# Kernel optimization log

Hardware: AMD Instinct MI355X
Metric: run time of the kernel (lower is better)

Reference implementation:

```python
import jax, jax.numpy as jnp
import numpy as np

COMMITMENT_COST = 0.25
KLD_SCALE = 1.0


def setup_inputs() -> dict:
    key = jax.random.key(0)
    k1, k2 = jax.random.split(key)
    z = jax.random.normal(k1, (8, 4096, 512), dtype=jnp.float32)
    embed_w = jax.random.normal(k2, (1024, 512), dtype=jnp.float32)
    return {"z": z, "embed_w": embed_w}


def reference(z, embed_w):
    bsz, s, d = z.shape
    flat = z.reshape(-1, d)  # [N, d]
    dist = (
        jnp.sum(flat * flat, axis=1, keepdims=True)
        - 2.0 * flat @ embed_w.T
        + jnp.sum(embed_w * embed_w, axis=1)[None, :]
    )
    ind = jnp.argmin(dist, axis=1).reshape(bsz, s)  # (-dist).max == dist.min
    z_q = embed_w[ind]  # codebook gather [bsz, s, d]
    sg = jax.lax.stop_gradient
    diff = COMMITMENT_COST * ((sg(z_q) - z) ** 2 + (z_q - sg(z)) ** 2)
    diff = diff * KLD_SCALE
    z_q = z + sg(z_q - z)  # straight-through estimator
    return z_q, diff, ind
```

## Files before the change

kernel.cpp:

```cpp
#include <hip/hip_runtime.h>
#include <math.h>


#define D_DIM   512
#define K_CODES 1024
#define N_TOK   32768

#define BM 128
#define BN 128
#define NKT 16

typedef __attribute__((ext_vector_type(8))) short bf16x8;
typedef __attribute__((ext_vector_type(4))) float f32x4;

__device__ __forceinline__ unsigned short bf16_rne(float f) {
    unsigned int u = __float_as_uint(f);
    return (unsigned short)((u + 0x7FFFu + ((u >> 16) & 1u)) >> 16);
}
__device__ __forceinline__ float bf16_to_f32(unsigned short b) {
    return __uint_as_float(((unsigned int)b) << 16);
}

#define GLOAD16(gp, lp)                                                        \
    __builtin_amdgcn_global_load_lds(                                          \
        (const __attribute__((address_space(1))) void*)(gp),                   \
        (__attribute__((address_space(3))) void*)(lp), 16, 0, 0)

__global__ __launch_bounds__(256) void vq_zsplit(const float* __restrict__ z,
                                                 unsigned short* __restrict__ zhi,
                                                 unsigned short* __restrict__ zlo) {
    const int tid = blockIdx.x * 256 + threadIdx.x;
    const float4* z4 = (const float4*)z;
    ushort4* h4 = (ushort4*)zhi;
    ushort4* l4 = (ushort4*)zlo;
#pragma unroll
    for (int g = 0; g < 8; ++g) {
        const size_t i = (size_t)g * 524288 + tid;
        float4 v = z4[i];
        float f[4] = {v.x, v.y, v.z, v.w};
        unsigned short hb[4], lb[4];
#pragma unroll
        for (int j = 0; j < 4; ++j) {
            hb[j] = bf16_rne(f[j]);
            lb[j] = bf16_rne(f[j] - bf16_to_f32(hb[j]));
        }
        h4[i] = make_ushort4(hb[0], hb[1], hb[2], hb[3]);
        l4[i] = make_ushort4(lb[0], lb[1], lb[2], lb[3]);
    }
}

__global__ __launch_bounds__(256) void vq_prep(const float* __restrict__ ew,
                                               unsigned short* __restrict__ ehi,
                                               unsigned short* __restrict__ elo,
                                               float* __restrict__ e2) {
    const int wv = threadIdx.x >> 6, lane = threadIdx.x & 63;
    const int code = blockIdx.x * 4 + wv;
    const float* row = ew + (size_t)code * D_DIM;
    float s = 0.0f;
#pragma unroll
    for (int h = 0; h < 2; ++h) {
        const int c = h * 256 + lane * 4;
        float4 v = *(const float4*)(row + c);
        float f[4] = {v.x, v.y, v.z, v.w};
        unsigned short hb[4], lb[4];
#pragma unroll
        for (int j = 0; j < 4; ++j) {
            s = fmaf(f[j], f[j], s);
            hb[j] = bf16_rne(f[j]);
            lb[j] = bf16_rne(f[j] - bf16_to_f32(hb[j]));
        }
        *(ushort4*)(ehi + (size_t)code * D_DIM + c) = make_ushort4(hb[0], hb[1], hb[2], hb[3]);
        *(ushort4*)(elo + (size_t)code * D_DIM + c) = make_ushort4(lb[0], lb[1], lb[2], lb[3]);
    }
#pragma unroll
    for (int off = 32; off > 0; off >>= 1) s += __shfl_xor(s, off, 64);
    if (lane == 0) e2[code] = s;
}

__global__ __launch_bounds__(256, 2) void vq_gemm(
    const unsigned short* __restrict__ zhi, const unsigned short* __restrict__ zlo,
    const unsigned short* __restrict__ ehi, const unsigned short* __restrict__ elo,
    const float* __restrict__ e2, float* __restrict__ pv, float* __restrict__ pif) {
    __shared__ __align__(16) unsigned short lds[32768];
    const int AHI = 0, ALO = 4096, BHI = 8192, BLO = 12288;

    const int t = threadIdx.x, lane = t & 63, wv = t >> 6;
    const int b  = blockIdx.x;
    const int wg = (b & 7) * 256 + (b >> 3);
    const int mtile = wg >> 3, ntile = wg & 7;
    const int row0 = mtile * BM;
    const int c0g  = ntile * BN;

    const int idx0 = (wv * 2 + 0) * 64 + lane;
    const int idx1 = (wv * 2 + 1) * 64 + lane;
    const int c_0 = idx0 >> 7, r_0 = idx0 & 127;
    const int c_1 = idx1 >> 7, r_1 = idx1 & 127;
    const size_t zo0 = (size_t)(row0 + r_0) * D_DIM + c_0 * 8;
    const size_t zo1 = (size_t)(row0 + r_1) * D_DIM + c_1 * 8;
    const size_t eo0 = (size_t)(c0g + r_0) * D_DIM + c_0 * 8;
    const size_t eo1 = (size_t)(c0g + r_1) * D_DIM + c_1 * 8;
    const int l0 = (wv * 2 + 0) * 512;
    const int l1 = (wv * 2 + 1) * 512;

    const int wr = wv >> 1, wc = wv & 1;
    const int lm = lane & 15, lk = lane >> 4;

    f32x4 acc[4][4];
    const f32x4 zero4 = {0.f, 0.f, 0.f, 0.f};
#pragma unroll
    for (int i = 0; i < 4; ++i)
#pragma unroll
        for (int j = 0; j < 4; ++j) acc[i][j] = zero4;

    auto stage = [&](int kt, int bufo) {
        const int ko = kt * 32;
        GLOAD16(zhi + zo0 + ko, &lds[bufo + AHI + l0]);
        GLOAD16(zhi + zo1 + ko, &lds[bufo + AHI + l1]);
        GLOAD16(zlo + zo0 + ko, &lds[bufo + ALO + l0]);
        GLOAD16(zlo + zo1 + ko, &lds[bufo + ALO + l1]);
        GLOAD16(ehi + eo0 + ko, &lds[bufo + BHI + l0]);
        GLOAD16(ehi + eo1 + ko, &lds[bufo + BHI + l1]);
        GLOAD16(elo + eo0 + ko, &lds[bufo + BLO + l0]);
        GLOAD16(elo + eo1 + ko, &lds[bufo + BLO + l1]);
    };

    auto compute = [&](int bufo) {
        bf16x8 ah[4], al[4], bh[4], bl[4];
#pragma unroll
        for (int mi = 0; mi < 4; ++mi) {
            const int s = (lk * 128 + wr * 64 + mi * 16 + lm) * 8;
            ah[mi] = *(const bf16x8*)&lds[bufo + AHI + s];
            al[mi] = *(const bf16x8*)&lds[bufo + ALO + s];
        }
#pragma unroll
        for (int nj = 0; nj < 4; ++nj) {
            const int s = (lk * 128 + wc * 64 + nj * 16 + lm) * 8;
            bh[nj] = *(const bf16x8*)&lds[bufo + BHI + s];
            bl[nj] = *(const bf16x8*)&lds[bufo + BLO + s];
        }
        __builtin_amdgcn_s_setprio(1);
#pragma unroll
        for (int mi = 0; mi < 4; ++mi)
#pragma unroll
            for (int nj = 0; nj < 4; ++nj)
                acc[mi][nj] = __builtin_amdgcn_mfma_f32_16x16x32_bf16(
                    ah[mi], bh[nj], acc[mi][nj], 0, 0, 0);
#pragma unroll
        for (int mi = 0; mi < 4; ++mi)
#pragma unroll
            for (int nj = 0; nj < 4; ++nj)
                acc[mi][nj] = __builtin_amdgcn_mfma_f32_16x16x32_bf16(
                    ah[mi], bl[nj], acc[mi][nj], 0, 0, 0);
#pragma unroll
        for (int mi = 0; mi < 4; ++mi)
#pragma unroll
            for (int nj = 0; nj < 4; ++nj)
                acc[mi][nj] = __builtin_amdgcn_mfma_f32_16x16x32_bf16(
                    al[mi], bh[nj], acc[mi][nj], 0, 0, 0);
        __builtin_amdgcn_s_setprio(0);
    };

    stage(0, 0);
    stage(1, 16384);

    for (int kt = 0; kt < NKT - 1; ++kt) {
        const int bufo = (kt & 1) * 16384;
        asm volatile("s_waitcnt vmcnt(8)" ::: "memory");
        __builtin_amdgcn_s_barrier();
        __builtin_amdgcn_sched_barrier(0);
        compute(bufo);
        __builtin_amdgcn_sched_barrier(0);
        __builtin_amdgcn_s_barrier();
        if (kt + 2 < NKT) stage(kt + 2, bufo);
    }
    {
        const int bufo = ((NKT - 1) & 1) * 16384;
        asm volatile("s_waitcnt vmcnt(0)" ::: "memory");
        __builtin_amdgcn_s_barrier();
        __builtin_amdgcn_sched_barrier(0);
        compute(bufo);
    }

    float best[16], bidx[16];
#pragma unroll
    for (int i = 0; i < 16; ++i) { best[i] = INFINITY; bidx[i] = 0.f; }
#pragma unroll
    for (int nj = 0; nj < 4; ++nj) {
        const int cloc = wc * 64 + nj * 16 + lm;
        const float e2v = e2[c0g + cloc];
#pragma unroll
        for (int mi = 0; mi < 4; ++mi)
#pragma unroll
            for (int r = 0; r < 4; ++r) {
                const float sc = fmaf(-2.0f, acc[mi][nj][r], e2v);
                const int bi = mi * 4 + r;
                if (sc < best[bi]) { best[bi] = sc; bidx[bi] = (float)(c0g + cloc); }
            }
    }
#pragma unroll
    for (int off = 1; off < 16; off <<= 1) {
#pragma unroll
        for (int bi = 0; bi < 16; ++bi) {
            float v2 = __shfl_xor(best[bi], off, 64);
            float i2 = __shfl_xor(bidx[bi], off, 64);
            if (v2 < best[bi] || (v2 == best[bi] && i2 < bidx[bi])) {
                best[bi] = v2; bidx[bi] = i2;
            }
        }
    }
    __syncthreads();
    float* sv = (float*)lds;
    float* si = sv + 256;
    if (lm == 0) {
#pragma unroll
        for (int mi = 0; mi < 4; ++mi)
#pragma unroll
            for (int r = 0; r < 4; ++r) {
                const int rl = wr * 64 + mi * 16 + lk * 4 + r;
                sv[wc * 128 + rl] = best[mi * 4 + r];
                si[wc * 128 + rl] = bidx[mi * 4 + r];
            }
    }
    __syncthreads();
    if (t < 128) {
        float v0 = sv[t], i0 = si[t];
        float v1 = sv[128 + t], i1 = si[128 + t];
        if (v1 < v0 || (v1 == v0 && i1 < i0)) { v0 = v1; i0 = i1; }
        pv [(size_t)ntile * N_TOK + row0 + t] = v0;
        pif[(size_t)ntile * N_TOK + row0 + t] = i0;
    }
}

__global__ __launch_bounds__(256) void vq_out_kernel(
    const float* __restrict__ z, const float* __restrict__ ew,
    const float* __restrict__ pv, const float* __restrict__ pif,
    float* __restrict__ indf, float* __restrict__ zq, float* __restrict__ diff) {
    const int w    = threadIdx.x >> 6;
    const int lane = threadIdx.x & 63;
    const int row  = blockIdx.x * 4 + w;

    float v = INFINITY, ix = 0.f;
    if (lane < 8) {
        v  = pv [(size_t)lane * N_TOK + row];
        ix = pif[(size_t)lane * N_TOK + row];
    }
#pragma unroll
    for (int off = 1; off < 8; off <<= 1) {
        float v2 = __shfl_xor(v, off, 64);
        float i2 = __shfl_xor(ix, off, 64);
        if (v2 < v || (v2 == v && i2 < ix)) { v = v2; ix = i2; }
    }
    const float ixb = __shfl(ix, 0, 64);
    const int c = (int)ixb;
    if (lane == 0) indf[row] = ixb;

    const float4* z4 = (const float4*)&z[(size_t)row * D_DIM];
    const float4* e4 = (const float4*)&ew[(size_t)c * D_DIM];
    float4* q4 = (float4*)&zq[(size_t)row * D_DIM];
    float4* d4 = (float4*)&diff[(size_t)row * D_DIM];

#pragma unroll
    for (int vv = 0; vv < 2; ++vv) {
        const int i = vv * 64 + lane;
        const float4 zv = z4[i];
        const float4 ev = e4[i];
        float4 qv, dv;
        float ax = ev.x - zv.x, ay = ev.y - zv.y, az = ev.z - zv.z, aw = ev.w - zv.w;
        qv.x = zv.x + ax; qv.y = zv.y + ay; qv.z = zv.z + az; qv.w = zv.w + aw;
        dv.x = 0.5f * (ax * ax); dv.y = 0.5f * (ay * ay);
        dv.z = 0.5f * (az * az); dv.w = 0.5f * (aw * aw);
        q4[i] = qv;
        d4[i] = dv;
    }
}

extern "C" void kernel_launch(void* const* d_in, const int* in_sizes, int n_in,
                              void* d_out, int out_size, void* d_ws, size_t ws_size,
                              hipStream_t stream) {
    const float* z  = (const float*)d_in[0];
    const float* ew = (const float*)d_in[1];
    float* out  = (float*)d_out;
    float* zq   = out;
    float* diff = out + (size_t)N_TOK * D_DIM;
    float* indf = out + (size_t)2 * N_TOK * D_DIM;

    char* s0 = (char*)d_out;
    unsigned short* ehi = (unsigned short*)(s0);
    unsigned short* elo = (unsigned short*)(s0 + (1u << 20));
    float* e2  = (float*)(s0 + (2u << 20));
    unsigned short* zhi = (unsigned short*)diff;
    unsigned short* zlo = zhi + (size_t)N_TOK * D_DIM;
    float* pv  = (float*)d_ws;
    float* pif = (float*)d_ws + (size_t)8 * N_TOK;

    hipLaunchKernelGGL(vq_zsplit, dim3(2048),        dim3(256), 0, stream, z, zhi, zlo);
    hipLaunchKernelGGL(vq_prep,   dim3(K_CODES / 4), dim3(256), 0, stream, ew, ehi, elo, e2);
    hipLaunchKernelGGL(vq_gemm,   dim3(2048),        dim3(256), 0, stream,
                       zhi, zlo, ehi, elo, e2, pv, pif);
    hipLaunchKernelGGL(vq_out_kernel, dim3(N_TOK / 4), dim3(256), 0, stream,
                       z, ew, pv, pif, indf, zq, diff);
}
```

Measured before the change: 191.9 us.

## Enlarge GEMM tile to 256 rows with 8 waves and triple-buffered LDS pipeline

The distance GEMM block grows from 128x128 to 256x128 with 512 threads, so each codebook tile loaded into LDS is reused by twice as many token rows. The double-buffered loop with two barriers per k-step becomes a three-buffer rotation with one barrier, issuing the next-next stage before compute. This cuts global traffic for the codebook and removes a sync per iteration. In exchange it uses more LDS per block (144KB at two blocks per CU) and halves the grid to 1024 blocks, which may lower occupancy or wave balance.

```diff
diff --git a/kernel.cpp b/kernel.cpp
--- a/kernel.cpp
+++ b/kernel.cpp
@@ -6,9 +6,10 @@
 #define K_CODES 1024
 #define N_TOK   32768
 
-#define BM 128
+#define BM 256
 #define BN 128
 #define NKT 16
+#define BUFU 24576
 
 typedef __attribute__((ext_vector_type(8))) short bf16x8;
 typedef __attribute__((ext_vector_type(4))) float f32x4;
@@ -77,30 +78,24 @@
     if (lane == 0) e2[code] = s;
 }
 
-__global__ __launch_bounds__(256, 2) void vq_gemm(
+__global__ __launch_bounds__(512, 2) void vq_gemm(
     const unsigned short* __restrict__ zhi, const unsigned short* __restrict__ zlo,
     const unsigned short* __restrict__ ehi, const unsigned short* __restrict__ elo,
     const float* __restrict__ e2, float* __restrict__ pv, float* __restrict__ pif) {
-    __shared__ __align__(16) unsigned short lds[32768];
-    const int AHI = 0, ALO = 4096, BHI = 8192, BLO = 12288;
+    __shared__ __align__(16) unsigned short lds[3 * BUFU];
+    const int AHI = 0, ALO = 8192, BHI = 16384, BLO = 20480;
 
     const int t = threadIdx.x, lane = t & 63, wv = t >> 6;
     const int b  = blockIdx.x;
-    const int wg = (b & 7) * 256 + (b >> 3);
+    const int wg = (b & 7) * 128 + (b >> 3);
     const int mtile = wg >> 3, ntile = wg & 7;
     const int row0 = mtile * BM;
     const int c0g  = ntile * BN;
 
-    const int idx0 = (wv * 2 + 0) * 64 + lane;
-    const int idx1 = (wv * 2 + 1) * 64 + lane;
-    const int c_0 = idx0 >> 7, r_0 = idx0 & 127;
-    const int c_1 = idx1 >> 7, r_1 = idx1 & 127;
-    const size_t zo0 = (size_t)(row0 + r_0) * D_DIM + c_0 * 8;
-    const size_t zo1 = (size_t)(row0 + r_1) * D_DIM + c_1 * 8;
-    const size_t eo0 = (size_t)(c0g + r_0) * D_DIM + c_0 * 8;
-    const size_t eo1 = (size_t)(c0g + r_1) * D_DIM + c_1 * 8;
-    const int l0 = (wv * 2 + 0) * 512;
-    const int l1 = (wv * 2 + 1) * 512;
+    const int acA = t >> 8;
+    const int arr = t & 255;
+    const int bcc = t >> 7;
+    const int brr = t & 127;
 
     const int wr = wv >> 1, wc = wv & 1;
     const int lm = lane & 15, lk = lane >> 4;
@@ -112,31 +107,34 @@
 #pragma unroll
         for (int j = 0; j < 4; ++j) acc[i][j] = zero4;
 
-    auto stage = [&](int kt, int bufo) {
+    auto stage = [&](int kt, int bo) {
         const int ko = kt * 32;
-        GLOAD16(zhi + zo0 + ko, &lds[bufo + AHI + l0]);
-        GLOAD16(zhi + zo1 + ko, &lds[bufo + AHI + l1]);
-        GLOAD16(zlo + zo0 + ko, &lds[bufo + ALO + l0]);
-        GLOAD16(zlo + zo1 + ko, &lds[bufo + ALO + l1]);
-        GLOAD16(ehi + eo0 + ko, &lds[bufo + BHI + l0]);
-        GLOAD16(ehi + eo1 + ko, &lds[bufo + BHI + l1]);
-        GLOAD16(elo + eo0 + ko, &lds[bufo + BLO + l0]);
-        GLOAD16(elo + eo1 + ko, &lds[bufo + BLO + l1]);
+#pragma unroll
+        for (int q = 0; q < 2; ++q) {
+            const size_t zo = (size_t)(row0 + arr) * D_DIM + ko + (q * 2 + acA) * 8;
+            const int sl = (q * 512 + t) * 8;
+            GLOAD16(zhi + zo, &lds[bo + AHI + sl]);
+            GLOAD16(zlo + zo, &lds[bo + ALO + sl]);
+        }
+        const size_t eo = (size_t)(c0g + brr) * D_DIM + ko + bcc * 8;
+        const int slb = t * 8;
+        GLOAD16(ehi + eo, &lds[bo + BHI + slb]);
+        GLOAD16(elo + eo, &lds[bo + BLO + slb]);
     };
 
-    auto compute = [&](int bufo) {
+    auto compute = [&](int bo) {
         bf16x8 ah[4], al[4], bh[4], bl[4];
 #pragma unroll
         for (int mi = 0; mi < 4; ++mi) {
-            const int s = (lk * 128 + wr * 64 + mi * 16 + lm) * 8;
-            ah[mi] = *(const bf16x8*)&lds[bufo + AHI + s];
-            al[mi] = *(const bf16x8*)&lds[bufo + ALO + s];
+            const int s = (lk * 256 + wr * 64 + mi * 16 + lm) * 8;
+            ah[mi] = *(const bf16x8*)&lds[bo + AHI + s];
+            al[mi] = *(const bf16x8*)&lds[bo + ALO + s];
         }
 #pragma unroll
         for (int nj = 0; nj < 4; ++nj) {
             const int s = (lk * 128 + wc * 64 + nj * 16 + lm) * 8;
-            bh[nj] = *(const bf16x8*)&lds[bufo + BHI + s];
-            bl[nj] = *(const bf16x8*)&lds[bufo + BLO + s];
+            bh[nj] = *(const bf16x8*)&lds[bo + BHI + s];
+            bl[nj] = *(const bf16x8*)&lds[bo + BLO + s];
         }
         __builtin_amdgcn_s_setprio(1);
 #pragma unroll
@@ -161,25 +159,19 @@
     };
 
     stage(0, 0);
-    stage(1, 16384);
-
+    stage(1, BUFU);
+
+    int boA = 0, boB = BUFU, boC = 2 * BUFU;
     for (int kt = 0; kt < NKT - 1; ++kt) {
-        const int bufo = (kt & 1) * 16384;
-        asm volatile("s_waitcnt vmcnt(8)" ::: "memory");
+        asm volatile("s_waitcnt vmcnt(6)" ::: "memory");
         __builtin_amdgcn_s_barrier();
-        __builtin_amdgcn_sched_barrier(0);
-        compute(bufo);
-        __builtin_amdgcn_sched_barrier(0);
-        __builtin_amdgcn_s_barrier();
-        if (kt + 2 < NKT) stage(kt + 2, bufo);
-    }
-    {
-        const int bufo = ((NKT - 1) & 1) * 16384;
-        asm volatile("s_waitcnt vmcnt(0)" ::: "memory");
-        __builtin_amdgcn_s_barrier();
-        __builtin_amdgcn_sched_barrier(0);
-        compute(bufo);
-    }
+        if (kt + 2 < NKT) stage(kt + 2, boC);
+        compute(boA);
+        const int tmp = boA; boA = boB; boB = boC; boC = tmp;
+    }
+    asm volatile("s_waitcnt vmcnt(0)" ::: "memory");
+    __builtin_amdgcn_s_barrier();
+    compute(boA);
 
     float best[16], bidx[16];
 #pragma unroll
@@ -210,21 +202,21 @@
     }
     __syncthreads();
     float* sv = (float*)lds;
-    float* si = sv + 256;
+    float* si = sv + 512;
     if (lm == 0) {
 #pragma unroll
         for (int mi = 0; mi < 4; ++mi)
 #pragma unroll
             for (int r = 0; r < 4; ++r) {
                 const int rl = wr * 64 + mi * 16 + lk * 4 + r;
-                sv[wc * 128 + rl] = best[mi * 4 + r];
-                si[wc * 128 + rl] = bidx[mi * 4 + r];
+                sv[wc * 256 + rl] = best[mi * 4 + r];
+                si[wc * 256 + rl] = bidx[mi * 4 + r];
             }
     }
     __syncthreads();
-    if (t < 128) {
+    if (t < 256) {
         float v0 = sv[t], i0 = si[t];
-        float v1 = sv[128 + t], i1 = si[128 + t];
+        float v1 = sv[256 + t], i1 = si[256 + t];
         if (v1 < v0 || (v1 == v0 && i1 < i0)) { v0 = v1; i0 = i1; }
         pv [(size_t)ntile * N_TOK + row0 + t] = v0;
         pif[(size_t)ntile * N_TOK + row0 + t] = i0;
@@ -295,7 +287,7 @@
 
     hipLaunchKernelGGL(vq_zsplit, dim3(2048),        dim3(256), 0, stream, z, zhi, zlo);
     hipLaunchKernelGGL(vq_prep,   dim3(K_CODES / 4), dim3(256), 0, stream, ew, ehi, elo, e2);
-    hipLaunchKernelGGL(vq_gemm,   dim3(2048),        dim3(256), 0, stream,
+    hipLaunchKernelGGL(vq_gemm,   dim3(N_TOK / BM * 8), dim3(512), 0, stream,
                        zhi, zlo, ehi, elo, e2, pv, pif);
     hipLaunchKernelGGL(vq_out_kernel, dim3(N_TOK / 4), dim3(256), 0, stream,
                        z, ew, pv, pif, indf, zq, diff);
```

Measured after the change: 249.8 us. +30.2%, slower.

## Switch VQ distance GEMM to 32x32x16 MFMA with smaller K-step tiles

Applied to the files above, without the earlier changes.

Replaces the 16x16x32 bf16 MFMA tiling with 32x32x16 MFMA and a 2x2 accumulator grid per wave. The K step per stage is halved (16 instead of 32), which halves the LDS footprint and allows launch bounds of 4 blocks per SM instead of 2. The argmin epilogue is rewritten for the 32x32 accumulator layout. The intent is higher MFMA efficiency and occupancy, at the cost of twice as many barrier-synchronised pipeline steps.

```diff
diff --git a/kernel.cpp b/kernel.cpp
--- a/kernel.cpp
+++ b/kernel.cpp
@@ -8,10 +8,11 @@
 
 #define BM 128
 #define BN 128
-#define NKT 16
+#define NKT 32
+#define BUFU 8192
 
 typedef __attribute__((ext_vector_type(8))) short bf16x8;
-typedef __attribute__((ext_vector_type(4))) float f32x4;
+typedef __attribute__((ext_vector_type(16))) float f32x16;
 
 __device__ __forceinline__ unsigned short bf16_rne(float f) {
     unsigned int u = __float_as_uint(f);
@@ -77,12 +78,11 @@
     if (lane == 0) e2[code] = s;
 }
 
-__global__ __launch_bounds__(256, 2) void vq_gemm(
+__global__ __launch_bounds__(256, 4) void vq_gemm(
     const unsigned short* __restrict__ zhi, const unsigned short* __restrict__ zlo,
     const unsigned short* __restrict__ ehi, const unsigned short* __restrict__ elo,
     const float* __restrict__ e2, float* __restrict__ pv, float* __restrict__ pif) {
-    __shared__ __align__(16) unsigned short lds[32768];
-    const int AHI = 0, ALO = 4096, BHI = 8192, BLO = 12288;
+    __shared__ __align__(16) unsigned short lds[2 * BUFU];
 
     const int t = threadIdx.x, lane = t & 63, wv = t >> 6;
     const int b  = blockIdx.x;
@@ -91,81 +91,73 @@
     const int row0 = mtile * BM;
     const int c0g  = ntile * BN;
 
-    const int idx0 = (wv * 2 + 0) * 64 + lane;
-    const int idx1 = (wv * 2 + 1) * 64 + lane;
-    const int c_0 = idx0 >> 7, r_0 = idx0 & 127;
-    const int c_1 = idx1 >> 7, r_1 = idx1 & 127;
-    const size_t zo0 = (size_t)(row0 + r_0) * D_DIM + c_0 * 8;
-    const size_t zo1 = (size_t)(row0 + r_1) * D_DIM + c_1 * 8;
-    const size_t eo0 = (size_t)(c0g + r_0) * D_DIM + c_0 * 8;
-    const size_t eo1 = (size_t)(c0g + r_1) * D_DIM + c_1 * 8;
-    const int l0 = (wv * 2 + 0) * 512;
-    const int l1 = (wv * 2 + 1) * 512;
+    const int kc_s = t >> 7;
+    const int rr_s = t & 127;
+    const size_t zo = (size_t)(row0 + rr_s) * D_DIM + kc_s * 8;
+    const size_t eo = (size_t)(c0g + rr_s) * D_DIM + kc_s * 8;
+    const int sl = t * 8;
 
     const int wr = wv >> 1, wc = wv & 1;
-    const int lm = lane & 15, lk = lane >> 4;
-
-    f32x4 acc[4][4];
-    const f32x4 zero4 = {0.f, 0.f, 0.f, 0.f};
-#pragma unroll
-    for (int i = 0; i < 4; ++i)
-#pragma unroll
-        for (int j = 0; j < 4; ++j) acc[i][j] = zero4;
+    const int l31 = lane & 31, kc = lane >> 5;
+
+    f32x16 acc[2][2];
+#pragma unroll
+    for (int i = 0; i < 2; ++i)
+#pragma unroll
+        for (int j = 0; j < 2; ++j)
+#pragma unroll
+            for (int r = 0; r < 16; ++r) acc[i][j][r] = 0.0f;
 
     auto stage = [&](int kt, int bufo) {
-        const int ko = kt * 32;
-        GLOAD16(zhi + zo0 + ko, &lds[bufo + AHI + l0]);
-        GLOAD16(zhi + zo1 + ko, &lds[bufo + AHI + l1]);
-        GLOAD16(zlo + zo0 + ko, &lds[bufo + ALO + l0]);
-        GLOAD16(zlo + zo1 + ko, &lds[bufo + ALO + l1]);
-        GLOAD16(ehi + eo0 + ko, &lds[bufo + BHI + l0]);
-        GLOAD16(ehi + eo1 + ko, &lds[bufo + BHI + l1]);
-        GLOAD16(elo + eo0 + ko, &lds[bufo + BLO + l0]);
-        GLOAD16(elo + eo1 + ko, &lds[bufo + BLO + l1]);
+        const int ko = kt * 16;
+        GLOAD16(zhi + zo + ko, &lds[bufo + 0    + sl]);
+        GLOAD16(zlo + zo + ko, &lds[bufo + 2048 + sl]);
+        GLOAD16(ehi + eo + ko, &lds[bufo + 4096 + sl]);
+        GLOAD16(elo + eo + ko, &lds[bufo + 6144 + sl]);
     };
 
     auto compute = [&](int bufo) {
-        bf16x8 ah[4], al[4], bh[4], bl[4];
-#pragma unroll
-        for (int mi = 0; mi < 4; ++mi) {
-            const int s = (lk * 128 + wr * 64 + mi * 16 + lm) * 8;
-            ah[mi] = *(const bf16x8*)&lds[bufo + AHI + s];
-            al[mi] = *(const bf16x8*)&lds[bufo + ALO + s];
-        }
-#pragma unroll
-        for (int nj = 0; nj < 4; ++nj) {
-            const int s = (lk * 128 + wc * 64 + nj * 16 + lm) * 8;
-            bh[nj] = *(const bf16x8*)&lds[bufo + BHI + s];
-            bl[nj] = *(const bf16x8*)&lds[bufo + BLO + s];
+        bf16x8 ah[2], al[2], bh[2], bl[2];
+#pragma unroll
+        for (int mi = 0; mi < 2; ++mi) {
+            const int s = (kc * 128 + wr * 64 + mi * 32 + l31) * 8;
+            ah[mi] = *(const bf16x8*)&lds[bufo + 0    + s];
+            al[mi] = *(const bf16x8*)&lds[bufo + 2048 + s];
+        }
+#pragma unroll
+        for (int nj = 0; nj < 2; ++nj) {
+            const int s = (kc * 128 + wc * 64 + nj * 32 + l31) * 8;
+            bh[nj] = *(const bf16x8*)&lds[bufo + 4096 + s];
+            bl[nj] = *(const bf16x8*)&lds[bufo + 6144 + s];
         }
         __builtin_amdgcn_s_setprio(1);
 #pragma unroll
-        for (int mi = 0; mi < 4; ++mi)
-#pragma unroll
-            for (int nj = 0; nj < 4; ++nj)
-                acc[mi][nj] = __builtin_amdgcn_mfma_f32_16x16x32_bf16(
+        for (int mi = 0; mi < 2; ++mi)
+#pragma unroll
+            for (int nj = 0; nj < 2; ++nj)
+                acc[mi][nj] = __builtin_amdgcn_mfma_f32_32x32x16_bf16(
                     ah[mi], bh[nj], acc[mi][nj], 0, 0, 0);
 #pragma unroll
-        for (int mi = 0; mi < 4; ++mi)
-#pragma unroll
-            for (int nj = 0; nj < 4; ++nj)
-                acc[mi][nj] = __builtin_amdgcn_mfma_f32_16x16x32_bf16(
+        for (int mi = 0; mi < 2; ++mi)
+#pragma unroll
+            for (int nj = 0; nj < 2; ++nj)
+                acc[mi][nj] = __builtin_amdgcn_mfma_f32_32x32x16_bf16(
                     ah[mi], bl[nj], acc[mi][nj], 0, 0, 0);
 #pragma unroll
-        for (int mi = 0; mi < 4; ++mi)
-#pragma unroll
-            for (int nj = 0; nj < 4; ++nj)
-                acc[mi][nj] = __builtin_amdgcn_mfma_f32_16x16x32_bf16(
+        for (int mi = 0; mi < 2; ++mi)
+#pragma unroll
+            for (int nj = 0; nj < 2; ++nj)
+                acc[mi][nj] = __builtin_amdgcn_mfma_f32_32x32x16_bf16(
                     al[mi], bh[nj], acc[mi][nj], 0, 0, 0);
         __builtin_amdgcn_s_setprio(0);
     };
 
     stage(0, 0);
-    stage(1, 16384);
+    stage(1, BUFU);
 
     for (int kt = 0; kt < NKT - 1; ++kt) {
-        const int bufo = (kt & 1) * 16384;
-        asm volatile("s_waitcnt vmcnt(8)" ::: "memory");
+        const int bufo = (kt & 1) * BUFU;
+        asm volatile("s_waitcnt vmcnt(4)" ::: "memory");
         __builtin_amdgcn_s_barrier();
         __builtin_amdgcn_sched_barrier(0);
         compute(bufo);
@@ -174,52 +166,52 @@
         if (kt + 2 < NKT) stage(kt + 2, bufo);
     }
     {
-        const int bufo = ((NKT - 1) & 1) * 16384;
+        const int bufo = ((NKT - 1) & 1) * BUFU;
         asm volatile("s_waitcnt vmcnt(0)" ::: "memory");
         __builtin_amdgcn_s_barrier();
         __builtin_amdgcn_sched_barrier(0);
         compute(bufo);
     }
 
-    float best[16], bidx[16];
-#pragma unroll
-    for (int i = 0; i < 16; ++i) { best[i] = INFINITY; bidx[i] = 0.f; }
-#pragma unroll
-    for (int nj = 0; nj < 4; ++nj) {
-        const int cloc = wc * 64 + nj * 16 + lm;
-        const float e2v = e2[c0g + cloc];
-#pragma unroll
-        for (int mi = 0; mi < 4; ++mi)
-#pragma unroll
-            for (int r = 0; r < 4; ++r) {
-                const float sc = fmaf(-2.0f, acc[mi][nj][r], e2v);
-                const int bi = mi * 4 + r;
-                if (sc < best[bi]) { best[bi] = sc; bidx[bi] = (float)(c0g + cloc); }
-            }
-    }
-#pragma unroll
-    for (int off = 1; off < 16; off <<= 1) {
-#pragma unroll
-        for (int bi = 0; bi < 16; ++bi) {
-            float v2 = __shfl_xor(best[bi], off, 64);
-            float i2 = __shfl_xor(bidx[bi], off, 64);
-            if (v2 < best[bi] || (v2 == best[bi] && i2 < bidx[bi])) {
-                best[bi] = v2; bidx[bi] = i2;
-            }
-        }
-    }
     __syncthreads();
     float* sv = (float*)lds;
     float* si = sv + 256;
-    if (lm == 0) {
-#pragma unroll
-        for (int mi = 0; mi < 4; ++mi)
-#pragma unroll
-            for (int r = 0; r < 4; ++r) {
-                const int rl = wr * 64 + mi * 16 + lk * 4 + r;
-                sv[wc * 128 + rl] = best[mi * 4 + r];
-                si[wc * 128 + rl] = bidx[mi * 4 + r];
+#pragma unroll
+    for (int mi = 0; mi < 2; ++mi) {
+        float best[16], bidx[16];
+#pragma unroll
+        for (int r = 0; r < 16; ++r) { best[r] = INFINITY; bidx[r] = 0.f; }
+#pragma unroll
+        for (int nj = 0; nj < 2; ++nj) {
+            const int cloc = wc * 64 + nj * 32 + l31;
+            const float e2v = e2[c0g + cloc];
+            const float cif = (float)(c0g + cloc);
+#pragma unroll
+            for (int r = 0; r < 16; ++r) {
+                const float sc = fmaf(-2.0f, acc[mi][nj][r], e2v);
+                if (sc < best[r]) { best[r] = sc; bidx[r] = cif; }
             }
+        }
+#pragma unroll
+        for (int off = 1; off < 32; off <<= 1) {
+#pragma unroll
+            for (int r = 0; r < 16; ++r) {
+                float v2 = __shfl_xor(best[r], off, 64);
+                float i2 = __shfl_xor(bidx[r], off, 64);
+                if (v2 < best[r] || (v2 == best[r] && i2 < bidx[r])) {
+                    best[r] = v2; bidx[r] = i2;
+                }
+            }
+        }
+        if (l31 == 0) {
+            const int hi4 = kc * 4;
+#pragma unroll
+            for (int r = 0; r < 16; ++r) {
+                const int rloc = wr * 64 + mi * 32 + (r & 3) + 8 * (r >> 2) + hi4;
+                sv[wc * 128 + rloc] = best[r];
+                si[wc * 128 + rloc] = bidx[r];
+            }
+        }
     }
     __syncthreads();
     if (t < 128) {
```

Result: slower. 230.3 us (+20.0%).

## Replace split-bf16 GEMM with single fp16 GEMM plus error-bounded fp32 refinement

Applied to the files above, without the earlier changes.

The three-pass bf16 hi/lo split GEMM becomes a single fp16 MFMA pass, with K-steps of 64 and half the staging loads. Each tile now keeps top-2 candidates per row, and a new refine kernel computes a rigorous error bound from residual norms and codebook norms. Rows whose winner is not clearly separated are re-evaluated exactly in fp32, either on the ambiguous candidate or on whole 128-code tiles. This removes two thirds of the MFMA work and the lo-plane traffic, at the cost of extra kernels and data-dependent fallback work. The fallback could be heavy if the bound is loose for normally distributed inputs.

```diff
diff --git a/kernel.cpp b/kernel.cpp
--- a/kernel.cpp
+++ b/kernel.cpp
@@ -8,81 +8,90 @@
 
 #define BM 128
 #define BN 128
-#define NKT 16
-
-typedef __attribute__((ext_vector_type(8))) short bf16x8;
+#define NKT 8
+#define BUFU 16384
+
+typedef __attribute__((ext_vector_type(8))) _Float16 f16x8;
 typedef __attribute__((ext_vector_type(4))) float f32x4;
-
-__device__ __forceinline__ unsigned short bf16_rne(float f) {
-    unsigned int u = __float_as_uint(f);
-    return (unsigned short)((u + 0x7FFFu + ((u >> 16) & 1u)) >> 16);
-}
-__device__ __forceinline__ float bf16_to_f32(unsigned short b) {
-    return __uint_as_float(((unsigned int)b) << 16);
-}
 
 #define GLOAD16(gp, lp)                                                        \
     __builtin_amdgcn_global_load_lds(                                          \
         (const __attribute__((address_space(1))) void*)(gp),                   \
         (__attribute__((address_space(3))) void*)(lp), 16, 0, 0)
 
-__global__ __launch_bounds__(256) void vq_zsplit(const float* __restrict__ z,
-                                                 unsigned short* __restrict__ zhi,
-                                                 unsigned short* __restrict__ zlo) {
-    const int tid = blockIdx.x * 256 + threadIdx.x;
-    const float4* z4 = (const float4*)z;
-    ushort4* h4 = (ushort4*)zhi;
-    ushort4* l4 = (ushort4*)zlo;
-#pragma unroll
-    for (int g = 0; g < 8; ++g) {
-        const size_t i = (size_t)g * 524288 + tid;
-        float4 v = z4[i];
-        float f[4] = {v.x, v.y, v.z, v.w};
-        unsigned short hb[4], lb[4];
-#pragma unroll
-        for (int j = 0; j < 4; ++j) {
-            hb[j] = bf16_rne(f[j]);
-            lb[j] = bf16_rne(f[j] - bf16_to_f32(hb[j]));
-        }
-        h4[i] = make_ushort4(hb[0], hb[1], hb[2], hb[3]);
-        l4[i] = make_ushort4(lb[0], lb[1], lb[2], lb[3]);
-    }
-}
-
-__global__ __launch_bounds__(256) void vq_prep(const float* __restrict__ ew,
-                                               unsigned short* __restrict__ ehi,
-                                               unsigned short* __restrict__ elo,
-                                               float* __restrict__ e2) {
+#define SB0 __builtin_amdgcn_sched_barrier(0)
+
+__device__ __forceinline__ bool lexlt(float v, float i, float w, float j) {
+    return v < w || (v == w && i < j);
+}
+__device__ __forceinline__ void top2_merge(float& v1, float& i1, float& v2, float& i2,
+                                           float w1, float j1, float w2, float j2) {
+    const bool bf = lexlt(w1, j1, v1, i1);
+    const float nv1 = bf ? w1 : v1, ni1 = bf ? j1 : i1;
+    const bool s = bf ? lexlt(v1, i1, w2, j2) : lexlt(w1, j1, v2, i2);
+    const float nv2 = bf ? (s ? v1 : w2) : (s ? w1 : v2);
+    const float ni2 = bf ? (s ? i1 : j2) : (s ? j1 : i2);
+    v1 = nv1; i1 = ni1; v2 = nv2; i2 = ni2;
+}
+
+__global__ __launch_bounds__(256) void vq_cvt16(const float* __restrict__ src,
+                                                _Float16* __restrict__ dst16,
+                                                float* __restrict__ n2,
+                                                float* __restrict__ r2o) {
     const int wv = threadIdx.x >> 6, lane = threadIdx.x & 63;
-    const int code = blockIdx.x * 4 + wv;
-    const float* row = ew + (size_t)code * D_DIM;
-    float s = 0.0f;
-#pragma unroll
-    for (int h = 0; h < 2; ++h) {
-        const int c = h * 256 + lane * 4;
-        float4 v = *(const float4*)(row + c);
-        float f[4] = {v.x, v.y, v.z, v.w};
-        unsigned short hb[4], lb[4];
-#pragma unroll
-        for (int j = 0; j < 4; ++j) {
-            s = fmaf(f[j], f[j], s);
-            hb[j] = bf16_rne(f[j]);
-            lb[j] = bf16_rne(f[j] - bf16_to_f32(hb[j]));
-        }
-        *(ushort4*)(ehi + (size_t)code * D_DIM + c) = make_ushort4(hb[0], hb[1], hb[2], hb[3]);
-        *(ushort4*)(elo + (size_t)code * D_DIM + c) = make_ushort4(lb[0], lb[1], lb[2], lb[3]);
-    }
-#pragma unroll
-    for (int off = 32; off > 0; off >>= 1) s += __shfl_xor(s, off, 64);
-    if (lane == 0) e2[code] = s;
-}
-
-__global__ __launch_bounds__(256, 2) void vq_gemm(
-    const unsigned short* __restrict__ zhi, const unsigned short* __restrict__ zlo,
-    const unsigned short* __restrict__ ehi, const unsigned short* __restrict__ elo,
-    const float* __restrict__ e2, float* __restrict__ pv, float* __restrict__ pif) {
-    __shared__ __align__(16) unsigned short lds[32768];
-    const int AHI = 0, ALO = 4096, BHI = 8192, BLO = 12288;
+    const int row = blockIdx.x * 4 + wv;
+    const float* rp = src + (size_t)row * D_DIM + lane * 8;
+    float4 a = *(const float4*)rp;
+    float4 b = *(const float4*)(rp + 4);
+    float s2 = 0.f, r2 = 0.f;
+    f16x8 h8;
+#pragma unroll
+    for (int j = 0; j < 8; ++j) {
+        const float x = j < 4 ? (&a.x)[j] : (&b.x)[j - 4];
+        const _Float16 h = (_Float16)x;
+        const float r = x - (float)h;
+        s2 = fmaf(x, x, s2);
+        r2 = fmaf(r, r, r2);
+        h8[j] = h;
+    }
+    *(f16x8*)(dst16 + (size_t)row * D_DIM + lane * 8) = h8;
+#pragma unroll
+    for (int off = 32; off > 0; off >>= 1) {
+        s2 += __shfl_xor(s2, off, 64);
+        r2 += __shfl_xor(r2, off, 64);
+    }
+    if (lane == 0) { n2[row] = s2; r2o[row] = r2; }
+}
+
+__global__ __launch_bounds__(256) void vq_maxes(const float* __restrict__ e2,
+                                                const float* __restrict__ el2,
+                                                float* __restrict__ maxs) {
+    const int t = threadIdx.x, wv = t >> 6, lane = t & 63;
+    float mE = 0.f, mEl = 0.f;
+#pragma unroll
+    for (int q = 0; q < 4; ++q) {
+        const int c = q * 256 + t;
+        mE  = fmaxf(mE,  sqrtf(e2[c]));
+        mEl = fmaxf(mEl, sqrtf(el2[c]));
+    }
+#pragma unroll
+    for (int off = 32; off > 0; off >>= 1) {
+        mE  = fmaxf(mE,  __shfl_xor(mE,  off, 64));
+        mEl = fmaxf(mEl, __shfl_xor(mEl, off, 64));
+    }
+    __shared__ float red[8];
+    if (lane == 0) { red[wv] = mE; red[4 + wv] = mEl; }
+    __syncthreads();
+    if (t == 0) {
+        maxs[0] = fmaxf(fmaxf(red[0], red[1]), fmaxf(red[2], red[3]));
+        maxs[1] = fmaxf(fmaxf(red[4], red[5]), fmaxf(red[6], red[7]));
+    }
+}
+
+__global__ __launch_bounds__(256, 2) void vq_gemm16(
+    const _Float16* __restrict__ z16, const _Float16* __restrict__ e16,
+    const float* __restrict__ e2, float4* __restrict__ cand) {
+    __shared__ __align__(16) unsigned short lds[2 * BUFU];
 
     const int t = threadIdx.x, lane = t & 63, wv = t >> 6;
     const int b  = blockIdx.x;
@@ -91,16 +100,9 @@
     const int row0 = mtile * BM;
     const int c0g  = ntile * BN;
 
-    const int idx0 = (wv * 2 + 0) * 64 + lane;
-    const int idx1 = (wv * 2 + 1) * 64 + lane;
-    const int c_0 = idx0 >> 7, r_0 = idx0 & 127;
-    const int c_1 = idx1 >> 7, r_1 = idx1 & 127;
-    const size_t zo0 = (size_t)(row0 + r_0) * D_DIM + c_0 * 8;
-    const size_t zo1 = (size_t)(row0 + r_1) * D_DIM + c_1 * 8;
-    const size_t eo0 = (size_t)(c0g + r_0) * D_DIM + c_0 * 8;
-    const size_t eo1 = (size_t)(c0g + r_1) * D_DIM + c_1 * 8;
-    const int l0 = (wv * 2 + 0) * 512;
-    const int l1 = (wv * 2 + 1) * 512;
+    const int arow = t & 127, khalf = t >> 7;
+    const size_t zob = (size_t)(row0 + arow) * D_DIM + khalf * 8;
+    const size_t eob = (size_t)(c0g + arow) * D_DIM + khalf * 8;
 
     const int wr = wv >> 1, wc = wv & 1;
     const int lm = lane & 15, lk = lane >> 4;
@@ -113,146 +115,171 @@
         for (int j = 0; j < 4; ++j) acc[i][j] = zero4;
 
     auto stage = [&](int kt, int bufo) {
-        const int ko = kt * 32;
-        GLOAD16(zhi + zo0 + ko, &lds[bufo + AHI + l0]);
-        GLOAD16(zhi + zo1 + ko, &lds[bufo + AHI + l1]);
-        GLOAD16(zlo + zo0 + ko, &lds[bufo + ALO + l0]);
-        GLOAD16(zlo + zo1 + ko, &lds[bufo + ALO + l1]);
-        GLOAD16(ehi + eo0 + ko, &lds[bufo + BHI + l0]);
-        GLOAD16(ehi + eo1 + ko, &lds[bufo + BHI + l1]);
-        GLOAD16(elo + eo0 + ko, &lds[bufo + BLO + l0]);
-        GLOAD16(elo + eo1 + ko, &lds[bufo + BLO + l1]);
+        const int ko = kt * 64;
+#pragma unroll
+        for (int q = 0; q < 4; ++q) {
+            const int sl = (q * 256 + t) * 8;
+            GLOAD16(z16 + zob + ko + q * 16, &lds[bufo + sl]);
+            GLOAD16(e16 + eob + ko + q * 16, &lds[bufo + 8192 + sl]);
+        }
     };
 
     auto compute = [&](int bufo) {
-        bf16x8 ah[4], al[4], bh[4], bl[4];
-#pragma unroll
-        for (int mi = 0; mi < 4; ++mi) {
-            const int s = (lk * 128 + wr * 64 + mi * 16 + lm) * 8;
-            ah[mi] = *(const bf16x8*)&lds[bufo + AHI + s];
-            al[mi] = *(const bf16x8*)&lds[bufo + ALO + s];
+#pragma unroll
+        for (int ks = 0; ks < 2; ++ks) {
+            f16x8 af[4], bf[4];
+#pragma unroll
+            for (int mi = 0; mi < 4; ++mi)
+                af[mi] = *(const f16x8*)&lds[bufo + ((ks * 4 + lk) * 128 + wr * 64 + mi * 16 + lm) * 8];
+#pragma unroll
+            for (int nj = 0; nj < 4; ++nj)
+                bf[nj] = *(const f16x8*)&lds[bufo + 8192 + ((ks * 4 + lk) * 128 + wc * 64 + nj * 16 + lm) * 8];
+            __builtin_amdgcn_s_setprio(1);
+#pragma unroll
+            for (int mi = 0; mi < 4; ++mi)
+#pragma unroll
+                for (int nj = 0; nj < 4; ++nj)
+                    acc[mi][nj] = __builtin_amdgcn_mfma_f32_16x16x32_f16(
+                        af[mi], bf[nj], acc[mi][nj], 0, 0, 0);
+            __builtin_amdgcn_s_setprio(0);
         }
-#pragma unroll
-        for (int nj = 0; nj < 4; ++nj) {
-            const int s = (lk * 128 + wc * 64 + nj * 16 + lm) * 8;
-            bh[nj] = *(const bf16x8*)&lds[bufo + BHI + s];
-            bl[nj] = *(const bf16x8*)&lds[bufo + BLO + s];
-        }
-        __builtin_amdgcn_s_setprio(1);
-#pragma unroll
-        for (int mi = 0; mi < 4; ++mi)
-#pragma unroll
-            for (int nj = 0; nj < 4; ++nj)
-                acc[mi][nj] = __builtin_amdgcn_mfma_f32_16x16x32_bf16(
-                    ah[mi], bh[nj], acc[mi][nj], 0, 0, 0);
-#pragma unroll
-        for (int mi = 0; mi < 4; ++mi)
-#pragma unroll
-            for (int nj = 0; nj < 4; ++nj)
-                acc[mi][nj] = __builtin_amdgcn_mfma_f32_16x16x32_bf16(
-                    ah[mi], bl[nj], acc[mi][nj], 0, 0, 0);
-#pragma unroll
-        for (int mi = 0; mi < 4; ++mi)
-#pragma unroll
-            for (int nj = 0; nj < 4; ++nj)
-                acc[mi][nj] = __builtin_amdgcn_mfma_f32_16x16x32_bf16(
-                    al[mi], bh[nj], acc[mi][nj], 0, 0, 0);
-        __builtin_amdgcn_s_setprio(0);
     };
 
     stage(0, 0);
-    stage(1, 16384);
-
+    stage(1, BUFU);
     for (int kt = 0; kt < NKT - 1; ++kt) {
-        const int bufo = (kt & 1) * 16384;
+        const int bufo = (kt & 1) * BUFU;
         asm volatile("s_waitcnt vmcnt(8)" ::: "memory");
         __builtin_amdgcn_s_barrier();
-        __builtin_amdgcn_sched_barrier(0);
+        SB0;
         compute(bufo);
-        __builtin_amdgcn_sched_barrier(0);
+        SB0;
         __builtin_amdgcn_s_barrier();
         if (kt + 2 < NKT) stage(kt + 2, bufo);
     }
     {
-        const int bufo = ((NKT - 1) & 1) * 16384;
+        const int bufo = ((NKT - 1) & 1) * BUFU;
         asm volatile("s_waitcnt vmcnt(0)" ::: "memory");
         __builtin_amdgcn_s_barrier();
-        __builtin_amdgcn_sched_barrier(0);
+        SB0;
         compute(bufo);
     }
 
-    float best[16], bidx[16];
-#pragma unroll
-    for (int i = 0; i < 16; ++i) { best[i] = INFINITY; bidx[i] = 0.f; }
+    float e2v[4], cif[4];
 #pragma unroll
     for (int nj = 0; nj < 4; ++nj) {
         const int cloc = wc * 64 + nj * 16 + lm;
-        const float e2v = e2[c0g + cloc];
-#pragma unroll
-        for (int mi = 0; mi < 4; ++mi)
-#pragma unroll
-            for (int r = 0; r < 4; ++r) {
-                const float sc = fmaf(-2.0f, acc[mi][nj][r], e2v);
-                const int bi = mi * 4 + r;
-                if (sc < best[bi]) { best[bi] = sc; bidx[bi] = (float)(c0g + cloc); }
+        e2v[nj] = e2[c0g + cloc];
+        cif[nj] = (float)(c0g + cloc);
+    }
+    __syncthreads();
+    float* svv = (float*)lds;
+#pragma unroll
+    for (int mi = 0; mi < 4; ++mi) {
+#pragma unroll
+        for (int r = 0; r < 4; ++r) {
+            float v1 = INFINITY, i1 = INFINITY, v2 = INFINITY, i2 = INFINITY;
+#pragma unroll
+            for (int nj = 0; nj < 4; ++nj) {
+                const float v = fmaf(-2.0f, acc[mi][nj][r], e2v[nj]);
+                const float ci = cif[nj];
+                if (lexlt(v, ci, v1, i1)) { v2 = v1; i2 = i1; v1 = v; i1 = ci; }
+                else if (lexlt(v, ci, v2, i2)) { v2 = v; i2 = ci; }
             }
-    }
-#pragma unroll
-    for (int off = 1; off < 16; off <<= 1) {
-#pragma unroll
-        for (int bi = 0; bi < 16; ++bi) {
-            float v2 = __shfl_xor(best[bi], off, 64);
-            float i2 = __shfl_xor(bidx[bi], off, 64);
-            if (v2 < best[bi] || (v2 == best[bi] && i2 < bidx[bi])) {
-                best[bi] = v2; bidx[bi] = i2;
+#pragma unroll
+            for (int off = 1; off < 16; off <<= 1) {
+                const float w1 = __shfl_xor(v1, off, 64), j1 = __shfl_xor(i1, off, 64);
+                const float w2 = __shfl_xor(v2, off, 64), j2 = __shfl_xor(i2, off, 64);
+                top2_merge(v1, i1, v2, i2, w1, j1, w2, j2);
+            }
+            if (lm == 0) {
+                const int rl = wr * 64 + mi * 16 + lk * 4 + r;
+                float* p = &svv[(wc * 128 + rl) * 4];
+                p[0] = v1; p[1] = i1; p[2] = v2; p[3] = i2;
             }
         }
     }
     __syncthreads();
-    float* sv = (float*)lds;
-    float* si = sv + 256;
-    if (lm == 0) {
-#pragma unroll
-        for (int mi = 0; mi < 4; ++mi)
-#pragma unroll
-            for (int r = 0; r < 4; ++r) {
-                const int rl = wr * 64 + mi * 16 + lk * 4 + r;
-                sv[wc * 128 + rl] = best[mi * 4 + r];
-                si[wc * 128 + rl] = bidx[mi * 4 + r];
-            }
-    }
-    __syncthreads();
     if (t < 128) {
-        float v0 = sv[t], i0 = si[t];
-        float v1 = sv[128 + t], i1 = si[128 + t];
-        if (v1 < v0 || (v1 == v0 && i1 < i0)) { v0 = v1; i0 = i1; }
-        pv [(size_t)ntile * N_TOK + row0 + t] = v0;
-        pif[(size_t)ntile * N_TOK + row0 + t] = i0;
-    }
+        const float* pa = &svv[t * 4];
+        const float* pb = &svv[(128 + t) * 4];
+        float v1 = pa[0], i1 = pa[1], v2 = pa[2], i2 = pa[3];
+        top2_merge(v1, i1, v2, i2, pb[0], pb[1], pb[2], pb[3]);
+        cand[(size_t)ntile * N_TOK + row0 + t] = make_float4(v1, i1, v2, i2);
+    }
+}
+
+__global__ __launch_bounds__(256) void vq_refine(
+    const float4* __restrict__ cand, const float* __restrict__ z,
+    const float* __restrict__ ew, const float* __restrict__ e2,
+    const float* __restrict__ z2, const float* __restrict__ zl2,
+    const float* __restrict__ maxs, float* __restrict__ indf) {
+    const int wv = threadIdx.x >> 6, lane = threadIdx.x & 63;
+    const int row = blockIdx.x * 4 + wv;
+
+    float v1 = INFINITY, i1 = INFINITY, v2 = INFINITY, i2 = INFINITY;
+    if (lane < 8) {
+        const float4 cd = cand[(size_t)lane * N_TOK + row];
+        v1 = cd.x; i1 = cd.y; v2 = cd.z; i2 = cd.w;
+    }
+    float mv = v1, mi_ = i1;
+#pragma unroll
+    for (int off = 1; off < 64; off <<= 1) {
+        const float ov = __shfl_xor(mv, off, 64), oi = __shfl_xor(mi_, off, 64);
+        if (lexlt(ov, oi, mv, mi_)) { mv = ov; mi_ = oi; }
+    }
+    const float tau = 2.0f * (sqrtf(zl2[row]) * maxs[0]
+                              + 1.001f * sqrtf(z2[row]) * maxs[1]) + 0.25f;
+    const float w = mv + 2.0f * tau;
+
+    const unsigned long long m1 = __ballot((lane < 8) && (v1 <= w));
+    const unsigned long long m2 = __ballot((lane < 8) && (v2 <= w));
+    if (m2 == 0 && __popcll(m1) == 1) {
+        if (lane == 0) indf[row] = mi_;
+        return;
+    }
+
+    const float* zp = z + (size_t)row * D_DIM + lane * 8;
+    const float4 za = *(const float4*)zp;
+    const float4 zb = *(const float4*)(zp + 4);
+    float bs = INFINITY, bi = INFINITY;
+
+    auto evalc = [&](int c) {
+        const float* ep = ew + (size_t)c * D_DIM + lane * 8;
+        const float4 ea = *(const float4*)ep;
+        const float4 eb = *(const float4*)(ep + 4);
+        float d = 0.f;
+        d = fmaf(za.x, ea.x, d); d = fmaf(za.y, ea.y, d);
+        d = fmaf(za.z, ea.z, d); d = fmaf(za.w, ea.w, d);
+        d = fmaf(zb.x, eb.x, d); d = fmaf(zb.y, eb.y, d);
+        d = fmaf(zb.z, eb.z, d); d = fmaf(zb.w, eb.w, d);
+#pragma unroll
+        for (int off = 1; off < 64; off <<= 1) d += __shfl_xor(d, off, 64);
+        const float s = fmaf(-2.0f, d, e2[c]);
+        const float ci = (float)c;
+        if (lexlt(s, ci, bs, bi)) { bs = s; bi = ci; }
+    };
+
+    for (int j = 0; j < 8; ++j) {
+        const float v2j = __shfl(v2, j, 64);
+        if (v2j <= w) {
+            for (int c = j * 128; c < j * 128 + 128; ++c) evalc(c);
+        } else {
+            const float v1j = __shfl(v1, j, 64);
+            if (v1j <= w) evalc((int)__shfl(i1, j, 64));
+        }
+    }
+    if (lane == 0) indf[row] = bi;
 }
 
 __global__ __launch_bounds__(256) void vq_out_kernel(
     const float* __restrict__ z, const float* __restrict__ ew,
-    const float* __restrict__ pv, const float* __restrict__ pif,
-    float* __restrict__ indf, float* __restrict__ zq, float* __restrict__ diff) {
+    const float* __restrict__ indf, float* __restrict__ zq,
+    float* __restrict__ diff) {
     const int w    = threadIdx.x >> 6;
     const int lane = threadIdx.x & 63;
     const int row  = blockIdx.x * 4 + w;
-
-    float v = INFINITY, ix = 0.f;
-    if (lane < 8) {
-        v  = pv [(size_t)lane * N_TOK + row];
-        ix = pif[(size_t)lane * N_TOK + row];
-    }
-#pragma unroll
-    for (int off = 1; off < 8; off <<= 1) {
-        float v2 = __shfl_xor(v, off, 64);
-        float i2 = __shfl_xor(ix, off, 64);
-        if (v2 < v || (v2 == v && i2 < ix)) { v = v2; ix = i2; }
-    }
-    const float ixb = __shfl(ix, 0, 64);
-    const int c = (int)ixb;
-    if (lane == 0) indf[row] = ixb;
+    const int c    = (int)indf[row];
 
     const float4* z4 = (const float4*)&z[(size_t)row * D_DIM];
     const float4* e4 = (const float4*)&ew[(size_t)c * D_DIM];
@@ -285,18 +312,21 @@
     float* indf = out + (size_t)2 * N_TOK * D_DIM;
 
     char* s0 = (char*)d_out;
-    unsigned short* ehi = (unsigned short*)(s0);
-    unsigned short* elo = (unsigned short*)(s0 + (1u << 20));
-    float* e2  = (float*)(s0 + (2u << 20));
-    unsigned short* zhi = (unsigned short*)diff;
-    unsigned short* zlo = zhi + (size_t)N_TOK * D_DIM;
-    float* pv  = (float*)d_ws;
-    float* pif = (float*)d_ws + (size_t)8 * N_TOK;
-
-    hipLaunchKernelGGL(vq_zsplit, dim3(2048),        dim3(256), 0, stream, z, zhi, zlo);
-    hipLaunchKernelGGL(vq_prep,   dim3(K_CODES / 4), dim3(256), 0, stream, ew, ehi, elo, e2);
-    hipLaunchKernelGGL(vq_gemm,   dim3(2048),        dim3(256), 0, stream,
-                       zhi, zlo, ehi, elo, e2, pv, pif);
+    _Float16* e16 = (_Float16*)s0;
+    float* e2   = (float*)(s0 + (1u << 20));
+    float* el2  = (float*)(s0 + (1u << 20) + 4096);
+    float* z2   = (float*)(s0 + (1u << 20) + 8192);
+    float* zl2  = (float*)(s0 + (1u << 20) + 8192 + 131072);
+    float* maxs = (float*)(s0 + (1u << 20) + 8192 + 262144);
+    float4* cand = (float4*)(s0 + (2u << 20));
+    _Float16* z16 = (_Float16*)diff;
+
+    hipLaunchKernelGGL(vq_cvt16, dim3(N_TOK / 4),   dim3(256), 0, stream, z, z16, z2, zl2);
+    hipLaunchKernelGGL(vq_cvt16, dim3(K_CODES / 4), dim3(256), 0, stream, ew, e16, e2, el2);
+    hipLaunchKernelGGL(vq_maxes, dim3(1),           dim3(256), 0, stream, e2, el2, maxs);
+    hipLaunchKernelGGL(vq_gemm16, dim3(2048),       dim3(256), 0, stream, z16, e16, e2, cand);
+    hipLaunchKernelGGL(vq_refine, dim3(N_TOK / 4),  dim3(256), 0, stream,
+                       cand, z, ew, e2, z2, zl2, maxs, indf);
     hipLaunchKernelGGL(vq_out_kernel, dim3(N_TOK / 4), dim3(256), 0, stream,
-                       z, ew, pv, pif, indf, zq, diff);
-}
+                       z, ew, indf, zq, diff);
+}
```

New measurement: 240.5 us. +25.3%, slower.
